# Kernel tuning notes

Hardware: AMD Instinct MI355X
Metric: run time of the kernel (lower is better)

## Reference

```python
import jax, jax.numpy as jnp
import numpy as np

N_NODES = 50000
N_EDGES = 800000
IN_CH = 128
HID = 64
MLP_HID = 128
EPS = 1e-5


def setup_inputs() -> dict:
    key = jax.random.key(0)
    ks = iter(jax.random.split(key, 32))
    d = {}
    d['x'] = jax.random.normal(next(ks), (N_NODES, IN_CH), dtype=jnp.float32)
    d['edge_index'] = jax.random.randint(next(ks), (2, N_EDGES), 0, N_NODES, dtype=jnp.int64)

    def lin(k, out_c, in_c, scale=None):
        s = scale if scale is not None else 1.0 / np.sqrt(in_c)
        return jax.random.uniform(k, (out_c, in_c), jnp.float32, -s, s)

    # layer 0: in->hid, with residual linear
    d['Wl0'] = lin(next(ks), HID, IN_CH); d['bl0'] = jnp.zeros((HID,), jnp.float32)
    d['Wr0'] = lin(next(ks), HID, IN_CH)
    d['g0'] = jnp.ones((HID,), jnp.float32); d['be0'] = jnp.zeros((HID,), jnp.float32)
    d['rW0'] = lin(next(ks), HID, IN_CH); d['rb0'] = jnp.zeros((HID,), jnp.float32)
    # layers 1,2: hid->hid, identity residual
    for i in (1, 2):
        d[f'Wl{i}'] = lin(next(ks), HID, HID); d[f'bl{i}'] = jnp.zeros((HID,), jnp.float32)
        d[f'Wr{i}'] = lin(next(ks), HID, HID)
        d[f'g{i}'] = jnp.ones((HID,), jnp.float32); d[f'be{i}'] = jnp.zeros((HID,), jnp.float32)
    # edge MLP: 2*HID -> MLP_HID -> MLP_HID -> 1
    d['W1'] = lin(next(ks), MLP_HID, 2 * HID); d['b1'] = jnp.zeros((MLP_HID,), jnp.float32)
    d['W2'] = lin(next(ks), MLP_HID, MLP_HID); d['b2'] = jnp.zeros((MLP_HID,), jnp.float32)
    d['W3'] = lin(next(ks), 1, MLP_HID); d['b3'] = jnp.zeros((1,), jnp.float32)
    return d


def _res_sage_layer(x, src, tgt, Wl, bl, Wr, g, be, rW=None, rb=None):
    # SAGEConv (mean aggr): out = lin_l(mean_{j in N(i)} x_j) + lin_r(x_i)
    msg = x[src]                                              # [E, C] gather
    agg = jax.ops.segment_sum(msg, tgt, num_segments=N_NODES)
    cnt = jax.ops.segment_sum(jnp.ones((msg.shape[0],), x.dtype), tgt, num_segments=N_NODES)
    mean = agg / jnp.maximum(cnt, 1.0)[:, None]
    out = mean @ Wl.T + bl + x @ Wr.T
    # BatchNorm (training-mode batch statistics, biased var)
    mu = out.mean(axis=0)
    var = out.var(axis=0)
    out = (out - mu) * jax.lax.rsqrt(var + EPS) * g + be
    out = jax.nn.relu(out)
    res = x @ rW.T + rb if rW is not None else x
    return out + res


def reference(x, edge_index, Wl0, bl0, Wr0, g0, be0, rW0, rb0,
              Wl1, bl1, Wr1, g1, be1, Wl2, bl2, Wr2, g2, be2,
              W1, b1, W2, b2, W3, b3):
    src, tgt = edge_index[0], edge_index[1]
    h = _res_sage_layer(x, src, tgt, Wl0, bl0, Wr0, g0, be0, rW0, rb0)
    h = _res_sage_layer(h, src, tgt, Wl1, bl1, Wr1, g1, be1)
    h = _res_sage_layer(h, src, tgt, Wl2, bl2, Wr2, g2, be2)
    edge_repr = jnp.concatenate([h[src], h[tgt]], axis=1)     # [E, 2*HID]
    z = jax.nn.relu(edge_repr @ W1.T + b1)                    # dropout: eval mode (identity)
    z = jax.nn.relu(z @ W2.T + b2)
    return z @ W3.T + b3                                      # [E, 1]
```

## Files before the change

### kernel.cpp

```cpp
#include <hip/hip_runtime.h>
#include <hip/hip_bf16.h>

#define NN 50000
#define NE 800000
#define HID 64
#define EPSV 1e-5f
#define NBLK 196

typedef __attribute__((ext_vector_type(8))) short bf16x8;
typedef __attribute__((ext_vector_type(4))) float f32x4;
typedef __attribute__((ext_vector_type(4))) int int4v;

__device__ __forceinline__ ushort f2b(float f) {
    union { __hip_bfloat16 b; ushort u; } c;
    c.b = __float2bfloat16(f);
    return c.u;
}
__device__ __forceinline__ float b2f(ushort u) {
    return __uint_as_float(((unsigned int)u) << 16);
}

__global__ void prep_w_kernel(const float* __restrict__ W1, const float* __restrict__ W2,
                              ushort* __restrict__ W1b, ushort* __restrict__ W2b) {
    int i = blockIdx.x * 256 + threadIdx.x;
    if (i < 16384) W1b[i] = f2b(W1[i]);
    else           W2b[i - 16384] = f2b(W2[i - 16384]);
}

__global__ void prep_nodew_kernel(
    const float* __restrict__ Wl0, const float* __restrict__ Wr0, const float* __restrict__ rW0,
    const float* __restrict__ Wl1, const float* __restrict__ Wr1,
    const float* __restrict__ Wl2, const float* __restrict__ Wr2,
    ushort* __restrict__ wnb)
{
    int i = blockIdx.x * 256 + threadIdx.x;
    if      (i < 8192)  wnb[i] = f2b(Wl0[i]);
    else if (i < 16384) wnb[i] = f2b(Wr0[i - 8192]);
    else if (i < 24576) wnb[i] = f2b(rW0[i - 16384]);
    else if (i < 28672) wnb[i] = f2b(Wl1[i - 24576]);
    else if (i < 32768) wnb[i] = f2b(Wr1[i - 28672]);
    else if (i < 36864) wnb[i] = f2b(Wl2[i - 32768]);
    else if (i < 40960) wnb[i] = f2b(Wr2[i - 36864]);
}

__global__ void xcvt_kernel(const float* __restrict__ x, ushort* __restrict__ xq) {
    int i = blockIdx.x * 256 + threadIdx.x;
    float4 a = *(const float4*)&x[i * 8];
    float4 b = *(const float4*)&x[i * 8 + 4];
    union { ushort u[8]; int4v v; } pk;
    pk.u[0] = f2b(a.x); pk.u[1] = f2b(a.y); pk.u[2] = f2b(a.z); pk.u[3] = f2b(a.w);
    pk.u[4] = f2b(b.x); pk.u[5] = f2b(b.y); pk.u[6] = f2b(b.z); pk.u[7] = f2b(b.w);
    *(int4v*)&xq[i * 8] = pk.v;
}

__global__ void count_kernel(const int* __restrict__ tgt, int* __restrict__ icnt) {
    int e = blockIdx.x * 256 + threadIdx.x;
    if (e < NE) atomicAdd(&icnt[tgt[e]], 1);
}

__global__ void scan1_kernel(const int* __restrict__ icnt, int* __restrict__ off,
                             int* __restrict__ bsum) {
    __shared__ int s[256];
    const int t = threadIdx.x;
    const int i = blockIdx.x * 256 + t;
    int v = (i < NN) ? icnt[i] : 0;
    s[t] = v;
    __syncthreads();
    for (int d = 1; d < 256; d <<= 1) {
        int x = (t >= d) ? s[t - d] : 0;
        __syncthreads();
        s[t] += x;
        __syncthreads();
    }
    if (i < NN) off[i] = s[t];
    if (t == 255) bsum[blockIdx.x] = s[255];
}

__global__ void scan2_kernel(const int* __restrict__ bsum, int* __restrict__ bpre) {
    __shared__ int s[256];
    const int t = threadIdx.x;
    int v = (t < NBLK) ? bsum[t] : 0;
    s[t] = v;
    __syncthreads();
    for (int d = 1; d < 256; d <<= 1) {
        int x = (t >= d) ? s[t - d] : 0;
        __syncthreads();
        s[t] += x;
        __syncthreads();
    }
    if (t < NBLK) bpre[t] = s[t] - v;
}

__global__ void scan3_kernel(const int* __restrict__ icnt, const int* __restrict__ bpre,
                             int* __restrict__ off, int* __restrict__ woff) {
    const int i = blockIdx.x * 256 + threadIdx.x;
    if (i < NN) {
        int e = off[i] - icnt[i] + bpre[blockIdx.x];
        off[i] = e;
        woff[i] = e;
        if (i == NN - 1) off[NN] = NE;
    }
}

__global__ void fill_kernel(const int* __restrict__ src, const int* __restrict__ tgt,
                            int* __restrict__ woff, int* __restrict__ ebuf) {
    int e = blockIdx.x * 256 + threadIdx.x;
    if (e < NE) {
        int p = atomicAdd(&woff[tgt[e]], 1);
        ebuf[p] = src[e];
    }
}

template<int K>
__global__ __launch_bounds__(256) void proj_mfma_kernel(
    const ushort* __restrict__ Ab,
    const ushort* __restrict__ w0, const ushort* __restrict__ w1,
    const ushort* __restrict__ w2,
    const float* __restrict__ bias1, const float* __restrict__ bias2,
    ushort* __restrict__ xb, float* __restrict__ pre, float* __restrict__ res)
{
    __shared__ float sC[128][65];
    const int tid = threadIdx.x;
    const int wv = tid >> 6, lane = tid & 63;
    const int l15 = lane & 15, l4 = lane >> 4;
    const int seg = blockIdx.y;
    const ushort* W = (seg == 0) ? w0 : ((seg == 1) ? w1 : w2);
    const int n0 = blockIdx.x * 128;
    constexpr int KS = K / 32;

    bf16x8 wf[4][KS];
    #pragma unroll
    for (int n = 0; n < 4; n++)
        #pragma unroll
        for (int ks = 0; ks < KS; ks++)
            wf[n][ks] = *(const bf16x8*)&W[(n * 16 + l15) * K + ks * 32 + l4 * 8];

    f32x4 acc[2][4];
    #pragma unroll
    for (int m = 0; m < 2; m++)
        #pragma unroll
        for (int n = 0; n < 4; n++)
            acc[m][n] = (f32x4){0.f, 0.f, 0.f, 0.f};

    #pragma unroll
    for (int m = 0; m < 2; m++) {
        int row = n0 + wv * 32 + m * 16 + l15;
        if (row > NN - 1) row = NN - 1;
        #pragma unroll
        for (int ks = 0; ks < KS; ks++) {
            bf16x8 a = *(const bf16x8*)&Ab[(long)row * K + ks * 32 + l4 * 8];
            #pragma unroll
            for (int n = 0; n < 4; n++)
                acc[m][n] = __builtin_amdgcn_mfma_f32_16x16x32_bf16(a, wf[n][ks], acc[m][n], 0, 0, 0);
        }
    }
    #pragma unroll
    for (int m = 0; m < 2; m++)
        #pragma unroll
        for (int n = 0; n < 4; n++)
            #pragma unroll
            for (int r = 0; r < 4; r++)
                sC[wv * 32 + m * 16 + l4 * 4 + r][n * 16 + l15] = acc[m][n][r];
    __syncthreads();

    const int r = tid >> 1, ch = (tid & 1) * 32;
    const int node = n0 + r;
    if (node < NN) {
        if (seg == 0) {
            #pragma unroll
            for (int g = 0; g < 4; g++) {
                union { ushort u[8]; int4v v; } pk;
                #pragma unroll
                for (int j = 0; j < 8; j++)
                    pk.u[j] = f2b(sC[r][ch + g * 8 + j]);
                *(int4v*)&xb[(long)node * 64 + ch + g * 8] = pk.v;
            }
        } else {
            float* O = (seg == 1) ? pre : res;
            const float* bp = (seg == 1) ? bias1 : bias2;
            #pragma unroll
            for (int g = 0; g < 8; g++) {
                int c = ch + g * 4;
                float4 v = make_float4(sC[r][c + 0] + bp[c + 0], sC[r][c + 1] + bp[c + 1],
                                       sC[r][c + 2] + bp[c + 2], sC[r][c + 3] + bp[c + 3]);
                *(float4*)&O[(long)node * 64 + c] = v;
            }
        }
    }
}

__global__ __launch_bounds__(256) void gather_bn_kernel(
    const int* __restrict__ off, const int* __restrict__ ebuf,
    const ushort* __restrict__ xb,
    float* __restrict__ vbase,
    float* __restrict__ bnsum, float* __restrict__ bnsq)
{
    __shared__ float r1[4][64], r2[4][64];
    const int lane = threadIdx.x & 63;
    const int wid = __builtin_amdgcn_readfirstlane(threadIdx.x >> 6);
    float s = 0.f, q = 0.f;
    for (int n = blockIdx.x * 4 + wid; n < NN; n += gridDim.x * 4) {
        const int a = off[n], b = off[n + 1];
        float a0 = 0.f, a1 = 0.f, a2 = 0.f, a3 = 0.f;
        int p = a;
        for (; p + 4 <= b; p += 4) {
            int s0 = ebuf[p], s1 = ebuf[p + 1], s2 = ebuf[p + 2], s3 = ebuf[p + 3];
            a0 += b2f(xb[(long)s0 * 64 + lane]);
            a1 += b2f(xb[(long)s1 * 64 + lane]);
            a2 += b2f(xb[(long)s2 * 64 + lane]);
            a3 += b2f(xb[(long)s3 * 64 + lane]);
        }
        for (; p < b; ++p) a0 += b2f(xb[(long)ebuf[p] * 64 + lane]);
        float acc = (a0 + a1) + (a2 + a3);
        float v = acc / fmaxf((float)(b - a), 1.f) + vbase[(long)n * 64 + lane];
        vbase[(long)n * 64 + lane] = v;
        s += v; q += v * v;
    }
    r1[wid][lane] = s; r2[wid][lane] = q;
    __syncthreads();
    if (threadIdx.x < 64) {
        s = r1[0][lane] + r1[1][lane] + r1[2][lane] + r1[3][lane];
        q = r2[0][lane] + r2[1][lane] + r2[2][lane] + r2[3][lane];
        atomicAdd(&bnsum[lane], s);
        atomicAdd(&bnsq[lane], q);
    }
}

__global__ void apply_bn_kernel(const float* __restrict__ vbase,
                                const float* __restrict__ resbase,
                                const float* __restrict__ bnsum, const float* __restrict__ bnsq,
                                const float* __restrict__ g, const float* __restrict__ be,
                                float* __restrict__ h, ushort* __restrict__ hb)
{
    const float inv_n = 1.0f / (float)NN;
    const int stride = gridDim.x * 256;
    for (int i = blockIdx.x * 256 + threadIdx.x; i < NN * 16; i += stride) {
        int n = i >> 4;
        int c0 = (i & 15) * 4;
        float sc[4], sh[4];
        #pragma unroll
        for (int j = 0; j < 4; j++) {
            int c = c0 + j;
            float mu = bnsum[c] * inv_n;
            float var = bnsq[c] * inv_n - mu * mu;
            float rstd = rsqrtf(var + EPSV);
            sc[j] = g[c] * rstd;
            sh[j] = be[c] - mu * sc[j];
        }
        float4 v = *(const float4*)&vbase[(long)n * 64 + c0];
        float4 r = *(const float4*)&resbase[(long)n * 64 + c0];
        float4 o;
        o.x = fmaxf(fmaf(v.x, sc[0], sh[0]), 0.f) + r.x;
        o.y = fmaxf(fmaf(v.y, sc[1], sh[1]), 0.f) + r.y;
        o.z = fmaxf(fmaf(v.z, sc[2], sh[2]), 0.f) + r.z;
        o.w = fmaxf(fmaf(v.w, sc[3], sh[3]), 0.f) + r.w;
        *(float4*)&h[(long)n * 64 + c0] = o;
        union { ushort u[4]; uint2 v2; } p;
        p.u[0] = f2b(o.x); p.u[1] = f2b(o.y); p.u[2] = f2b(o.z); p.u[3] = f2b(o.w);
        *(uint2*)&hb[(long)n * 64 + c0] = p.v2;
    }
}

#define NSTRIP 25000
#define EMG 256
#define ZSTR 136

#define GATHER(ss)                                                        \
    do {                                                                  \
        int e0g = (ss) * 32;                                              \
        _Pragma("unroll")                                                 \
        for (int m = 0; m < 2; m++) {                                     \
            int e = e0g + m * 16 + l15;                                   \
            const ushort* hs = hb + (long)src[e] * 64;                    \
            const ushort* ht = hb + (long)tgt[e] * 64;                    \
            ga[m][0] = *(const bf16x8*)&hs[l4 * 8];                       \
            ga[m][1] = *(const bf16x8*)&hs[32 + l4 * 8];                  \
            ga[m][2] = *(const bf16x8*)&ht[l4 * 8];                       \
            ga[m][3] = *(const bf16x8*)&ht[32 + l4 * 8];                  \
        }                                                                 \
    } while (0)

__global__ __launch_bounds__(512) void edge_mlp_wave_kernel(
    const ushort* __restrict__ hb,
    const int* __restrict__ src, const int* __restrict__ tgt,
    const ushort* __restrict__ W1b, const ushort* __restrict__ W2b,
    const float* __restrict__ b1, const float* __restrict__ b2,
    const float* __restrict__ W3, const float* __restrict__ b3,
    float* __restrict__ out)
{
    __shared__ ushort wlds[32768];
    __shared__ ushort z1[8][32 * ZSTR];

    const int tid = threadIdx.x;
    const int wid = tid >> 6, lane = tid & 63;
    const int l15 = lane & 15, l4 = lane >> 4;

    for (int c = tid; c < 4096; c += 512) {
        int layer = c >> 11, oc = (c >> 4) & 127, kc = c & 15;
        const ushort* Wsrc = layer ? W2b : W1b;
        int4v v = *(const int4v*)&Wsrc[oc * 128 + kc * 8];
        int byte = layer * 32768 + oc * 256 + ((kc * 16) ^ ((oc & 7) << 4));
        *(int4v*)((char*)wlds + byte) = v;
    }

    float b1v[8], b2v[8], w3v[8];
    #pragma unroll
    for (int n = 0; n < 8; n++) {
        int oc = n * 16 + l15;
        b1v[n] = b1[oc]; b2v[n] = b2[oc]; w3v[n] = W3[oc];
    }
    const float b3v = b3[0];

    const int bid = blockIdx.x;
    const int q = NSTRIP / EMG, r = NSTRIP % EMG;
    const int t0 = bid * q + (bid < r ? bid : r);
    const int nt = q + (bid < r ? 1 : 0);
    ushort* zw = z1[wid];

    bf16x8 ga[2][4];
    if (wid < nt) GATHER(t0 + wid);
    __syncthreads();

    for (int j = wid; j < nt; j += 8) {
        const int e0 = (t0 + j) * 32;

        f32x4 acc[2][8];
        #pragma unroll
        for (int m = 0; m < 2; m++)
            #pragma unroll
            for (int n = 0; n < 8; n++)
                acc[m][n] = (f32x4){b1v[n], b1v[n], b1v[n], b1v[n]};
        #pragma unroll
        for (int ks = 0; ks < 4; ks++) {
            bf16x8 wf[8];
            #pragma unroll
            for (int n = 0; n < 8; n++) {
                int oc = n * 16 + l15;
                int byte = oc * 256 + (((ks * 4 + l4) * 16) ^ ((oc & 7) << 4));
                wf[n] = *(const bf16x8*)((const char*)wlds + byte);
            }
            #pragma unroll
            for (int m = 0; m < 2; m++)
                #pragma unroll
                for (int n = 0; n < 8; n++)
                    acc[m][n] = __builtin_amdgcn_mfma_f32_16x16x32_bf16(ga[m][ks], wf[n], acc[m][n], 0, 0, 0);
        }
        #pragma unroll
        for (int m = 0; m < 2; m++)
            #pragma unroll
            for (int n = 0; n < 8; n++) {
                int col = n * 16 + l15;
                #pragma unroll
                for (int rr = 0; rr < 4; rr++)
                    zw[(m * 16 + l4 * 4 + rr) * ZSTR + col] = f2b(fmaxf(acc[m][n][rr], 0.f));
            }

        if (j + 8 < nt) GATHER(t0 + j + 8);

        f32x4 acc2[2][8];
        #pragma unroll
        for (int m = 0; m < 2; m++)
            #pragma unroll
            for (int n = 0; n < 8; n++)
                acc2[m][n] = (f32x4){b2v[n], b2v[n], b2v[n], b2v[n]};
        #pragma unroll
        for (int ks = 0; ks < 4; ks++) {
            bf16x8 wf[8];
            #pragma unroll
            for (int n = 0; n < 8; n++) {
                int oc = n * 16 + l15;
                int byte = 32768 + oc * 256 + (((ks * 4 + l4) * 16) ^ ((oc & 7) << 4));
                wf[n] = *(const bf16x8*)((const char*)wlds + byte);
            }
            bf16x8 a2[2];
            #pragma unroll
            for (int m = 0; m < 2; m++)
                a2[m] = *(const bf16x8*)&zw[(m * 16 + l15) * ZSTR + ks * 32 + l4 * 8];
            #pragma unroll
            for (int m = 0; m < 2; m++)
                #pragma unroll
                for (int n = 0; n < 8; n++)
                    acc2[m][n] = __builtin_amdgcn_mfma_f32_16x16x32_bf16(a2[m], wf[n], acc2[m][n], 0, 0, 0);
        }

        #pragma unroll
        for (int m = 0; m < 2; m++) {
            float sv[4];
            #pragma unroll
            for (int rr = 0; rr < 4; rr++) {
                float s = 0.f;
                #pragma unroll
                for (int n = 0; n < 8; n++)
                    s = fmaf(fmaxf(acc2[m][n][rr], 0.f), w3v[n], s);
                s += __shfl_xor(s, 1);
                s += __shfl_xor(s, 2);
                s += __shfl_xor(s, 4);
                s += __shfl_xor(s, 8);
                sv[rr] = s + b3v;
            }
            if (l15 == 0)
                *(float4*)&out[e0 + m * 16 + l4 * 4] =
                    make_float4(sv[0], sv[1], sv[2], sv[3]);
        }
    }
}

extern "C" void kernel_launch(void* const* d_in, const int* in_sizes, int n_in,
                              void* d_out, int out_size, void* d_ws, size_t ws_size,
                              hipStream_t stream)
{
    const float* x   = (const float*)d_in[0];
    const int*   ei  = (const int*)d_in[1];
    const int* src = ei;
    const int* tgt = ei + NE;
    const float* Wl0 = (const float*)d_in[2];
    const float* bl0 = (const float*)d_in[3];
    const float* Wr0 = (const float*)d_in[4];
    const float* g0  = (const float*)d_in[5];
    const float* be0 = (const float*)d_in[6];
    const float* rW0 = (const float*)d_in[7];
    const float* rb0 = (const float*)d_in[8];
    const float* Wl1 = (const float*)d_in[9];
    const float* bl1 = (const float*)d_in[10];
    const float* Wr1 = (const float*)d_in[11];
    const float* g1  = (const float*)d_in[12];
    const float* be1 = (const float*)d_in[13];
    const float* Wl2 = (const float*)d_in[14];
    const float* bl2 = (const float*)d_in[15];
    const float* Wr2 = (const float*)d_in[16];
    const float* g2  = (const float*)d_in[17];
    const float* be2 = (const float*)d_in[18];
    const float* W1  = (const float*)d_in[19];
    const float* b1  = (const float*)d_in[20];
    const float* W2  = (const float*)d_in[21];
    const float* b2  = (const float*)d_in[22];
    const float* W3  = (const float*)d_in[23];
    const float* b3  = (const float*)d_in[24];
    float* out = (float*)d_out;

    float* ws = (float*)d_ws;
    float*  pre  = ws;
    float*  res  = ws + 3200000;
    float*  hbuf = ws + 6400000;
    float*  bn   = ws + 9600000;
    float*  bnsum = bn, *bnsq = bn + 64;
    ushort* xb   = (ushort*)(ws + 9600256);
    ushort* hb   = (ushort*)(ws + 11200256);
    ushort* W1b  = (ushort*)(ws + 12800256);
    ushort* W2b  = W1b + 16384;
    int*    icnt = (int*)(ws + 12816640);
    int*    off  = icnt + 50000;
    int*    woff = off + 50001;
    int*    ebuf = woff + 50000;
    int*    bsum = ebuf + 800000;
    int*    bpre = bsum + 256;
    ushort* wnb  = (ushort*)(ws + 13767153);
    ushort* Wl0b = wnb;
    ushort* Wr0b = wnb + 8192;
    ushort* rW0b = wnb + 16384;
    ushort* Wl1b = wnb + 24576;
    ushort* Wr1b = wnb + 28672;
    ushort* Wl2b = wnb + 32768;
    ushort* Wr2b = wnb + 36864;
    ushort* xb16 = (ushort*)hbuf;

    prep_w_kernel<<<128, 256, 0, stream>>>(W1, W2, W1b, W2b);
    prep_nodew_kernel<<<160, 256, 0, stream>>>(Wl0, Wr0, rW0, Wl1, Wr1, Wl2, Wr2, wnb);
    xcvt_kernel<<<3125, 256, 0, stream>>>(x, xb16);
    hipMemsetAsync(icnt, 0, NN * sizeof(int), stream);
    count_kernel<<<NE / 256, 256, 0, stream>>>(tgt, icnt);
    scan1_kernel<<<NBLK, 256, 0, stream>>>(icnt, off, bsum);
    scan2_kernel<<<1, 256, 0, stream>>>(bsum, bpre);
    scan3_kernel<<<NBLK, 256, 0, stream>>>(icnt, bpre, off, woff);
    fill_kernel<<<NE / 256, 256, 0, stream>>>(src, tgt, woff, ebuf);

    dim3 g0g(391, 3), g12g(391, 2);

    hipMemsetAsync(bnsum, 0, 128 * sizeof(float), stream);
    proj_mfma_kernel<128><<<g0g, 256, 0, stream>>>(xb16, Wl0b, Wr0b, rW0b,
                                                   bl0, rb0, xb, pre, res);
    gather_bn_kernel<<<1024, 256, 0, stream>>>(off, ebuf, xb, pre, bnsum, bnsq);
    apply_bn_kernel<<<1024, 256, 0, stream>>>(pre, res, bnsum, bnsq, g0, be0, hbuf, hb);

    hipMemsetAsync(bnsum, 0, 128 * sizeof(float), stream);
    proj_mfma_kernel<64><<<g12g, 256, 0, stream>>>(hb, Wl1b, Wr1b, nullptr,
                                                   bl1, nullptr, xb, pre, res);
    gather_bn_kernel<<<1024, 256, 0, stream>>>(off, ebuf, xb, pre, bnsum, bnsq);
    apply_bn_kernel<<<1024, 256, 0, stream>>>(pre, hbuf, bnsum, bnsq, g1, be1, hbuf, hb);

    hipMemsetAsync(bnsum, 0, 128 * sizeof(float), stream);
    proj_mfma_kernel<64><<<g12g, 256, 0, stream>>>(hb, Wl2b, Wr2b, nullptr,
                                                   bl2, nullptr, xb, pre, res);
    gather_bn_kernel<<<1024, 256, 0, stream>>>(off, ebuf, xb, pre, bnsum, bnsq);
    apply_bn_kernel<<<1024, 256, 0, stream>>>(pre, hbuf, bnsum, bnsq, g2, be2, hbuf, hb);

    edge_mlp_wave_kernel<<<EMG, 512, 0, stream>>>(hb, src, tgt, W1b, W2b, b1, b2, W3, b3, out);
}
```

Measured before the change: 430.4 us.

## Fuse BN-apply into next layer projection and merge prep/scan launches

Merges the weight-conversion kernels and the memsets into one prep kernel, collapses the three-kernel scan into two, folds the fp32-to-bf16 conversion of x into the first projection, and fuses BatchNorm apply, ReLU and residual with the next layer's MFMA projection through a swizzled LDS tile. The aim is to cut kernel launches and to avoid writing hb and reading it back between layers. In exchange, apply_proj reads pre and writes pre in place across blocks, which is only safe because each block touches its own rows. It also loops the two weight segments serially inside a single block, which lowers parallelism compared with the previous 2D grid.

```diff
diff --git a/kernel.cpp b/kernel.cpp
--- a/kernel.cpp
+++ b/kernel.cpp
@@ -20,37 +20,26 @@
     return __uint_as_float(((unsigned int)u) << 16);
 }
 
-__global__ void prep_w_kernel(const float* __restrict__ W1, const float* __restrict__ W2,
-                              ushort* __restrict__ W1b, ushort* __restrict__ W2b) {
-    int i = blockIdx.x * 256 + threadIdx.x;
-    if (i < 16384) W1b[i] = f2b(W1[i]);
-    else           W2b[i - 16384] = f2b(W2[i - 16384]);
-}
-
-__global__ void prep_nodew_kernel(
+__global__ void prep_all_kernel(
+    const float* __restrict__ W1, const float* __restrict__ W2,
     const float* __restrict__ Wl0, const float* __restrict__ Wr0, const float* __restrict__ rW0,
     const float* __restrict__ Wl1, const float* __restrict__ Wr1,
     const float* __restrict__ Wl2, const float* __restrict__ Wr2,
-    ushort* __restrict__ wnb)
+    ushort* __restrict__ W1b, ushort* __restrict__ W2b,
+    ushort* __restrict__ wnb, int* __restrict__ icnt, float* __restrict__ bnbuf)
 {
     int i = blockIdx.x * 256 + threadIdx.x;
-    if      (i < 8192)  wnb[i] = f2b(Wl0[i]);
-    else if (i < 16384) wnb[i] = f2b(Wr0[i - 8192]);
-    else if (i < 24576) wnb[i] = f2b(rW0[i - 16384]);
-    else if (i < 28672) wnb[i] = f2b(Wl1[i - 24576]);
-    else if (i < 32768) wnb[i] = f2b(Wr1[i - 28672]);
-    else if (i < 36864) wnb[i] = f2b(Wl2[i - 32768]);
-    else if (i < 40960) wnb[i] = f2b(Wr2[i - 36864]);
-}
-
-__global__ void xcvt_kernel(const float* __restrict__ x, ushort* __restrict__ xq) {
-    int i = blockIdx.x * 256 + threadIdx.x;
-    float4 a = *(const float4*)&x[i * 8];
-    float4 b = *(const float4*)&x[i * 8 + 4];
-    union { ushort u[8]; int4v v; } pk;
-    pk.u[0] = f2b(a.x); pk.u[1] = f2b(a.y); pk.u[2] = f2b(a.z); pk.u[3] = f2b(a.w);
-    pk.u[4] = f2b(b.x); pk.u[5] = f2b(b.y); pk.u[6] = f2b(b.z); pk.u[7] = f2b(b.w);
-    *(int4v*)&xq[i * 8] = pk.v;
+    if      (i < 16384)  W1b[i] = f2b(W1[i]);
+    else if (i < 32768)  W2b[i - 16384] = f2b(W2[i - 16384]);
+    else if (i < 40960)  wnb[i - 32768] = f2b(Wl0[i - 32768]);
+    else if (i < 49152)  wnb[i - 32768] = f2b(Wr0[i - 40960]);
+    else if (i < 57344)  wnb[i - 32768] = f2b(rW0[i - 49152]);
+    else if (i < 61440)  wnb[i - 32768] = f2b(Wl1[i - 57344]);
+    else if (i < 65536)  wnb[i - 32768] = f2b(Wr1[i - 61440]);
+    else if (i < 69632)  wnb[i - 32768] = f2b(Wl2[i - 65536]);
+    else if (i < 73728)  wnb[i - 32768] = f2b(Wr2[i - 69632]);
+    else if (i < 123728) icnt[i - 73728] = 0;
+    else if (i < 124112) bnbuf[i - 123728] = 0.f;
 }
 
 __global__ void count_kernel(const int* __restrict__ tgt, int* __restrict__ icnt) {
@@ -58,7 +47,7 @@
     if (e < NE) atomicAdd(&icnt[tgt[e]], 1);
 }
 
-__global__ void scan1_kernel(const int* __restrict__ icnt, int* __restrict__ off,
+__global__ void scanA_kernel(const int* __restrict__ icnt, int* __restrict__ off,
                              int* __restrict__ bsum) {
     __shared__ int s[256];
     const int t = threadIdx.x;
@@ -76,26 +65,22 @@
     if (t == 255) bsum[blockIdx.x] = s[255];
 }
 
-__global__ void scan2_kernel(const int* __restrict__ bsum, int* __restrict__ bpre) {
-    __shared__ int s[256];
-    const int t = threadIdx.x;
-    int v = (t < NBLK) ? bsum[t] : 0;
-    s[t] = v;
-    __syncthreads();
-    for (int d = 1; d < 256; d <<= 1) {
-        int x = (t >= d) ? s[t - d] : 0;
+__global__ void scanB_kernel(const int* __restrict__ icnt, const int* __restrict__ bsum,
+                             int* __restrict__ off, int* __restrict__ woff) {
+    __shared__ int red[256];
+    const int t = threadIdx.x, bid = blockIdx.x;
+    int s = 0;
+    for (int j = t; j < bid; j += 256) s += bsum[j];
+    red[t] = s;
+    __syncthreads();
+    for (int d = 128; d > 0; d >>= 1) {
+        if (t < d) red[t] += red[t + d];
         __syncthreads();
-        s[t] += x;
-        __syncthreads();
-    }
-    if (t < NBLK) bpre[t] = s[t] - v;
-}
-
-__global__ void scan3_kernel(const int* __restrict__ icnt, const int* __restrict__ bpre,
-                             int* __restrict__ off, int* __restrict__ woff) {
-    const int i = blockIdx.x * 256 + threadIdx.x;
+    }
+    const int bpre = red[0];
+    const int i = bid * 256 + t;
     if (i < NN) {
-        int e = off[i] - icnt[i] + bpre[blockIdx.x];
+        int e = off[i] - icnt[i] + bpre;
         off[i] = e;
         woff[i] = e;
         if (i == NN - 1) off[NN] = NE;
@@ -111,9 +96,8 @@
     }
 }
 
-template<int K>
-__global__ __launch_bounds__(256) void proj_mfma_kernel(
-    const ushort* __restrict__ Ab,
+__global__ __launch_bounds__(256) void proj0_mfma_kernel(
+    const float* __restrict__ x,
     const ushort* __restrict__ w0, const ushort* __restrict__ w1,
     const ushort* __restrict__ w2,
     const float* __restrict__ bias1, const float* __restrict__ bias2,
@@ -126,14 +110,13 @@
     const int seg = blockIdx.y;
     const ushort* W = (seg == 0) ? w0 : ((seg == 1) ? w1 : w2);
     const int n0 = blockIdx.x * 128;
-    constexpr int KS = K / 32;
-
-    bf16x8 wf[4][KS];
+
+    bf16x8 wf[4][4];
     #pragma unroll
     for (int n = 0; n < 4; n++)
         #pragma unroll
-        for (int ks = 0; ks < KS; ks++)
-            wf[n][ks] = *(const bf16x8*)&W[(n * 16 + l15) * K + ks * 32 + l4 * 8];
+        for (int ks = 0; ks < 4; ks++)
+            wf[n][ks] = *(const bf16x8*)&W[(n * 16 + l15) * 128 + ks * 32 + l4 * 8];
 
     f32x4 acc[2][4];
     #pragma unroll
@@ -147,11 +130,16 @@
         int row = n0 + wv * 32 + m * 16 + l15;
         if (row > NN - 1) row = NN - 1;
         #pragma unroll
-        for (int ks = 0; ks < KS; ks++) {
-            bf16x8 a = *(const bf16x8*)&Ab[(long)row * K + ks * 32 + l4 * 8];
+        for (int ks = 0; ks < 4; ks++) {
+            const float* ap = &x[(long)row * 128 + ks * 32 + l4 * 8];
+            float4 f0 = *(const float4*)ap;
+            float4 f1 = *(const float4*)(ap + 4);
+            union { ushort u[8]; bf16x8 b; } a;
+            a.u[0] = f2b(f0.x); a.u[1] = f2b(f0.y); a.u[2] = f2b(f0.z); a.u[3] = f2b(f0.w);
+            a.u[4] = f2b(f1.x); a.u[5] = f2b(f1.y); a.u[6] = f2b(f1.z); a.u[7] = f2b(f1.w);
             #pragma unroll
             for (int n = 0; n < 4; n++)
-                acc[m][n] = __builtin_amdgcn_mfma_f32_16x16x32_bf16(a, wf[n][ks], acc[m][n], 0, 0, 0);
+                acc[m][n] = __builtin_amdgcn_mfma_f32_16x16x32_bf16(a.b, wf[n][ks], acc[m][n], 0, 0, 0);
         }
     }
     #pragma unroll
@@ -226,11 +214,136 @@
     }
 }
 
-__global__ void apply_bn_kernel(const float* __restrict__ vbase,
-                                const float* __restrict__ resbase,
-                                const float* __restrict__ bnsum, const float* __restrict__ bnsq,
-                                const float* __restrict__ g, const float* __restrict__ be,
-                                float* __restrict__ h, ushort* __restrict__ hb)
+__global__ __launch_bounds__(256) void apply_proj_kernel(
+    const float* __restrict__ vIn,
+    const float* __restrict__ resb,
+    const float* __restrict__ bnsum, const float* __restrict__ bnsq,
+    const float* __restrict__ g, const float* __restrict__ be,
+    float* __restrict__ hout,
+    const ushort* __restrict__ Wl, const ushort* __restrict__ Wr,
+    const float* __restrict__ bias,
+    ushort* __restrict__ xb, float* __restrict__ preOut)
+{
+    __shared__ float scs[64], shs[64];
+    __shared__ ushort tile[128 * 72];
+    __shared__ float sC[128][65];
+    const int tid = threadIdx.x;
+    const int n0 = blockIdx.x * 128;
+    const int wv = tid >> 6, lane = tid & 63;
+    const int l15 = lane & 15, l4 = lane >> 4;
+
+    if (tid < 64) {
+        const float inv_n = 1.0f / (float)NN;
+        float mu = bnsum[tid] * inv_n;
+        float var = bnsq[tid] * inv_n - mu * mu;
+        float rstd = rsqrtf(var + EPSV);
+        float sc = g[tid] * rstd;
+        scs[tid] = sc;
+        shs[tid] = be[tid] - mu * sc;
+    }
+    __syncthreads();
+
+    {
+        const int rloc = tid >> 1;
+        const int n = n0 + rloc;
+        const int ch = (tid & 1) * 32;
+        if (n < NN) {
+            #pragma unroll
+            for (int gq = 0; gq < 4; gq++) {
+                int c = ch + gq * 8;
+                float4 v0 = *(const float4*)&vIn[(long)n * 64 + c];
+                float4 v1 = *(const float4*)&vIn[(long)n * 64 + c + 4];
+                float4 r0 = *(const float4*)&resb[(long)n * 64 + c];
+                float4 r1 = *(const float4*)&resb[(long)n * 64 + c + 4];
+                float o[8];
+                o[0] = fmaxf(fmaf(v0.x, scs[c + 0], shs[c + 0]), 0.f) + r0.x;
+                o[1] = fmaxf(fmaf(v0.y, scs[c + 1], shs[c + 1]), 0.f) + r0.y;
+                o[2] = fmaxf(fmaf(v0.z, scs[c + 2], shs[c + 2]), 0.f) + r0.z;
+                o[3] = fmaxf(fmaf(v0.w, scs[c + 3], shs[c + 3]), 0.f) + r0.w;
+                o[4] = fmaxf(fmaf(v1.x, scs[c + 4], shs[c + 4]), 0.f) + r1.x;
+                o[5] = fmaxf(fmaf(v1.y, scs[c + 5], shs[c + 5]), 0.f) + r1.y;
+                o[6] = fmaxf(fmaf(v1.z, scs[c + 6], shs[c + 6]), 0.f) + r1.z;
+                o[7] = fmaxf(fmaf(v1.w, scs[c + 7], shs[c + 7]), 0.f) + r1.w;
+                *(float4*)&hout[(long)n * 64 + c]     = make_float4(o[0], o[1], o[2], o[3]);
+                *(float4*)&hout[(long)n * 64 + c + 4] = make_float4(o[4], o[5], o[6], o[7]);
+                union { ushort u[8]; int4v v; } pk;
+                #pragma unroll
+                for (int j = 0; j < 8; j++) pk.u[j] = f2b(o[j]);
+                int byte = rloc * 144 + ((c * 2) ^ ((rloc & 7) << 4));
+                *(int4v*)((char*)tile + byte) = pk.v;
+            }
+        }
+    }
+    __syncthreads();
+
+    for (int seg = 0; seg < 2; seg++) {
+        const ushort* W = seg ? Wr : Wl;
+        bf16x8 wf[4][2];
+        #pragma unroll
+        for (int n = 0; n < 4; n++)
+            #pragma unroll
+            for (int ks = 0; ks < 2; ks++)
+                wf[n][ks] = *(const bf16x8*)&W[(n * 16 + l15) * 64 + ks * 32 + l4 * 8];
+
+        f32x4 acc[2][4];
+        #pragma unroll
+        for (int m = 0; m < 2; m++)
+            #pragma unroll
+            for (int n = 0; n < 4; n++)
+                acc[m][n] = (f32x4){0.f, 0.f, 0.f, 0.f};
+
+        #pragma unroll
+        for (int m = 0; m < 2; m++) {
+            const int row = wv * 32 + m * 16 + l15;
+            #pragma unroll
+            for (int ks = 0; ks < 2; ks++) {
+                int byte = row * 144 + ((((ks * 32 + l4 * 8) * 2)) ^ ((row & 7) << 4));
+                bf16x8 a = *(const bf16x8*)((const char*)tile + byte);
+                #pragma unroll
+                for (int n = 0; n < 4; n++)
+                    acc[m][n] = __builtin_amdgcn_mfma_f32_16x16x32_bf16(a, wf[n][ks], acc[m][n], 0, 0, 0);
+            }
+        }
+        #pragma unroll
+        for (int m = 0; m < 2; m++)
+            #pragma unroll
+            for (int n = 0; n < 4; n++)
+                #pragma unroll
+                for (int r = 0; r < 4; r++)
+                    sC[wv * 32 + m * 16 + l4 * 4 + r][n * 16 + l15] = acc[m][n][r];
+        __syncthreads();
+
+        const int r = tid >> 1, ch = (tid & 1) * 32;
+        const int node = n0 + r;
+        if (node < NN) {
+            if (seg == 0) {
+                #pragma unroll
+                for (int gq = 0; gq < 4; gq++) {
+                    union { ushort u[8]; int4v v; } pk;
+                    #pragma unroll
+                    for (int j = 0; j < 8; j++)
+                        pk.u[j] = f2b(sC[r][ch + gq * 8 + j]);
+                    *(int4v*)&xb[(long)node * 64 + ch + gq * 8] = pk.v;
+                }
+            } else {
+                #pragma unroll
+                for (int gq = 0; gq < 8; gq++) {
+                    int c = ch + gq * 4;
+                    float4 v = make_float4(sC[r][c + 0] + bias[c + 0], sC[r][c + 1] + bias[c + 1],
+                                           sC[r][c + 2] + bias[c + 2], sC[r][c + 3] + bias[c + 3]);
+                    *(float4*)&preOut[(long)node * 64 + c] = v;
+                }
+            }
+        }
+        __syncthreads();
+    }
+}
+
+__global__ void apply_final_kernel(const float* __restrict__ vIn,
+                                   const float* __restrict__ resb,
+                                   const float* __restrict__ bnsum, const float* __restrict__ bnsq,
+                                   const float* __restrict__ g, const float* __restrict__ be,
+                                   ushort* __restrict__ hb)
 {
     const float inv_n = 1.0f / (float)NN;
     const int stride = gridDim.x * 256;
@@ -247,16 +360,13 @@
             sc[j] = g[c] * rstd;
             sh[j] = be[c] - mu * sc[j];
         }
-        float4 v = *(const float4*)&vbase[(long)n * 64 + c0];
-        float4 r = *(const float4*)&resbase[(long)n * 64 + c0];
-        float4 o;
-        o.x = fmaxf(fmaf(v.x, sc[0], sh[0]), 0.f) + r.x;
-        o.y = fmaxf(fmaf(v.y, sc[1], sh[1]), 0.f) + r.y;
-        o.z = fmaxf(fmaf(v.z, sc[2], sh[2]), 0.f) + r.z;
-        o.w = fmaxf(fmaf(v.w, sc[3], sh[3]), 0.f) + r.w;
-        *(float4*)&h[(long)n * 64 + c0] = o;
+        float4 v = *(const float4*)&vIn[(long)n * 64 + c0];
+        float4 r = *(const float4*)&resb[(long)n * 64 + c0];
         union { ushort u[4]; uint2 v2; } p;
-        p.u[0] = f2b(o.x); p.u[1] = f2b(o.y); p.u[2] = f2b(o.z); p.u[3] = f2b(o.w);
+        p.u[0] = f2b(fmaxf(fmaf(v.x, sc[0], sh[0]), 0.f) + r.x);
+        p.u[1] = f2b(fmaxf(fmaf(v.y, sc[1], sh[1]), 0.f) + r.y);
+        p.u[2] = f2b(fmaxf(fmaf(v.z, sc[2], sh[2]), 0.f) + r.z);
+        p.u[3] = f2b(fmaxf(fmaf(v.w, sc[3], sh[3]), 0.f) + r.w);
         *(uint2*)&hb[(long)n * 64 + c0] = p.v2;
     }
 }
@@ -442,8 +552,6 @@
     float*  pre  = ws;
     float*  res  = ws + 3200000;
     float*  hbuf = ws + 6400000;
-    float*  bn   = ws + 9600000;
-    float*  bnsum = bn, *bnsq = bn + 64;
     ushort* xb   = (ushort*)(ws + 9600256);
     ushort* hb   = (ushort*)(ws + 11200256);
     ushort* W1b  = (ushort*)(ws + 12800256);
@@ -453,8 +561,7 @@
     int*    woff = off + 50001;
     int*    ebuf = woff + 50000;
     int*    bsum = ebuf + 800000;
-    int*    bpre = bsum + 256;
-    ushort* wnb  = (ushort*)(ws + 13767153);
+    ushort* wnb  = (ushort*)(ws + 13766912);
     ushort* Wl0b = wnb;
     ushort* Wr0b = wnb + 8192;
     ushort* rW0b = wnb + 16384;
@@ -462,37 +569,31 @@
     ushort* Wr1b = wnb + 28672;
     ushort* Wl2b = wnb + 32768;
     ushort* Wr2b = wnb + 36864;
-    ushort* xb16 = (ushort*)hbuf;
-
-    prep_w_kernel<<<128, 256, 0, stream>>>(W1, W2, W1b, W2b);
-    prep_nodew_kernel<<<160, 256, 0, stream>>>(Wl0, Wr0, rW0, Wl1, Wr1, Wl2, Wr2, wnb);
-    xcvt_kernel<<<3125, 256, 0, stream>>>(x, xb16);
-    hipMemsetAsync(icnt, 0, NN * sizeof(int), stream);
+    float*  bn   = ws + 13787392;
+    float*  bnsum0 = bn,       *bnsq0 = bn + 64;
+    float*  bnsum1 = bn + 128, *bnsq1 = bn + 192;
+    float*  bnsum2 = bn + 256, *bnsq2 = bn + 320;
+
+    prep_all_kernel<<<485, 256, 0, stream>>>(W1, W2, Wl0, Wr0, rW0, Wl1, Wr1, Wl2, Wr2,
+                                             W1b, W2b, wnb, icnt, bn);
     count_kernel<<<NE / 256, 256, 0, stream>>>(tgt, icnt);
-    scan1_kernel<<<NBLK, 256, 0, stream>>>(icnt, off, bsum);
-    scan2_kernel<<<1, 256, 0, stream>>>(bsum, bpre);
-    scan3_kernel<<<NBLK, 256, 0, stream>>>(icnt, bpre, off, woff);
+    scanA_kernel<<<NBLK, 256, 0, stream>>>(icnt, off, bsum);
+    scanB_kernel<<<NBLK, 256, 0, stream>>>(icnt, bsum, off, woff);
     fill_kernel<<<NE / 256, 256, 0, stream>>>(src, tgt, woff, ebuf);
 
-    dim3 g0g(391, 3), g12g(391, 2);
-
-    hipMemsetAsync(bnsum, 0, 128 * sizeof(float), stream);
-    proj_mfma_kernel<128><<<g0g, 256, 0, stream>>>(xb16, Wl0b, Wr0b, rW0b,
-                                                   bl0, rb0, xb, pre, res);
-    gather_bn_kernel<<<1024, 256, 0, stream>>>(off, ebuf, xb, pre, bnsum, bnsq);
-    apply_bn_kernel<<<1024, 256, 0, stream>>>(pre, res, bnsum, bnsq, g0, be0, hbuf, hb);
-
-    hipMemsetAsync(bnsum, 0, 128 * sizeof(float), stream);
-    proj_mfma_kernel<64><<<g12g, 256, 0, stream>>>(hb, Wl1b, Wr1b, nullptr,
-                                                   bl1, nullptr, xb, pre, res);
-    gather_bn_kernel<<<1024, 256, 0, stream>>>(off, ebuf, xb, pre, bnsum, bnsq);
-    apply_bn_kernel<<<1024, 256, 0, stream>>>(pre, hbuf, bnsum, bnsq, g1, be1, hbuf, hb);
-
-    hipMemsetAsync(bnsum, 0, 128 * sizeof(float), stream);
-    proj_mfma_kernel<64><<<g12g, 256, 0, stream>>>(hb, Wl2b, Wr2b, nullptr,
-                                                   bl2, nullptr, xb, pre, res);
-    gather_bn_kernel<<<1024, 256, 0, stream>>>(off, ebuf, xb, pre, bnsum, bnsq);
-    apply_bn_kernel<<<1024, 256, 0, stream>>>(pre, hbuf, bnsum, bnsq, g2, be2, hbuf, hb);
+    dim3 g0g(391, 3);
+    proj0_mfma_kernel<<<g0g, 256, 0, stream>>>(x, Wl0b, Wr0b, rW0b, bl0, rb0, xb, pre, res);
+    gather_bn_kernel<<<1024, 256, 0, stream>>>(off, ebuf, xb, pre, bnsum0, bnsq0);
+
+    apply_proj_kernel<<<391, 256, 0, stream>>>(pre, res, bnsum0, bnsq0, g0, be0,
+                                               hbuf, Wl1b, Wr1b, bl1, xb, pre);
+    gather_bn_kernel<<<1024, 256, 0, stream>>>(off, ebuf, xb, pre, bnsum1, bnsq1);
+
+    apply_proj_kernel<<<391, 256, 0, stream>>>(pre, hbuf, bnsum1, bnsq1, g1, be1,
+                                               hbuf, Wl2b, Wr2b, bl2, xb, pre);
+    gather_bn_kernel<<<1024, 256, 0, stream>>>(off, ebuf, xb, pre, bnsum2, bnsq2);
+
+    apply_final_kernel<<<1024, 256, 0, stream>>>(pre, hbuf, bnsum2, bnsq2, g2, be2, hb);
 
     edge_mlp_wave_kernel<<<EMG, 512, 0, stream>>>(hb, src, tgt, W1b, W2b, b1, b2, W3, b3, out);
 }
```

After: 416.9 us. -3.1%, faster.
